# Kernel optimization log

Hardware: AMD Instinct MI355X
Metric: run time of the kernel (lower is better)

Reference implementation:

```python
import jax, jax.numpy as jnp
import numpy as np

KS = (3, 3)   # kernel_size
ST = (1, 1)   # stride
PD = (1, 1)   # padding
EPS = 1e-5


def unfold(x):
    """im2col matching torch.nn.Unfold: [B,C,H,W] -> [B, C*kh*kw, L] with (c,kh,kw) channel order, L row-major."""
    kh, kw = KS; sh, sw = ST; ph, pw = PD
    x = jnp.pad(x, ((0, 0), (0, 0), (ph, ph), (pw, pw)))
    B, C, H, W = x.shape
    Ho = (H - kh) // sh + 1
    Wo = (W - kw) // sw + 1
    I = (jnp.arange(Ho) * sh)[:, None, None, None] + jnp.arange(kh)[None, :, None, None]
    J = (jnp.arange(Wo) * sw)[None, None, :, None] + jnp.arange(kw)[None, None, None, :]
    p = x[:, :, I, J]  # [B, C, Ho, kh, Wo, kw]
    return p.transpose(0, 1, 3, 5, 2, 4).reshape(B, C * kh * kw, Ho * Wo)


def fold(cols, x_shape):
    """torch.nn.Fold is exactly the adjoint of Unfold (overlap-add)."""
    _, vjp = jax.vjp(unfold, jnp.zeros(x_shape, cols.dtype))
    return vjp(cols)[0]


def setup_inputs() -> dict:
    key = jax.random.key(0)
    k = jax.random.split(key, 6)
    B, C, H, W = 16, 64, 64, 64
    Cout, K = 64, KS[0] * KS[1]
    return {
        "x_mag": jax.random.uniform(k[0], (B, C, H, W), jnp.float32),
        "x_ang": jax.random.normal(k[1], (B, C, H, W), jnp.float32),
        "w_mag": jax.random.uniform(k[2], (C, K), jnp.float32),
        "w_ang": jax.random.uniform(k[3], (C, K), jnp.float32),
        "w1": jax.random.uniform(k[4], (C, K), jnp.float32),
        "w2": jax.random.uniform(k[5], (Cout, C), jnp.float32),
    }


def reference(x_mag, x_ang, w_mag, w_ang, w1, w2):
    B, C, H, W = x_mag.shape
    K = KS[0] * KS[1]
    Cout = w2.shape[0]
    Ho = (H + 2 * PD[0] - KS[0]) // ST[0] + 1
    Wo = (W + 2 * PD[1] - KS[1]) // ST[1] + 1

    # outer layer: unfold, mix with normalized weights, fold back (overlap-add)
    nws_mag = w_mag ** 2 / jnp.sum(w_mag ** 2)   # _normalize_weights_squared
    nw_ang = w_ang / jnp.sum(w_ang ** 2)         # _normalize_weights
    cm = unfold(x_mag).reshape(B, C, K, -1) + nws_mag[None, :, :, None]
    ca = unfold(x_ang).reshape(B, C, K, -1) * nw_ang[None, :, :, None]
    fm = fold(cm.reshape(B, C * K, -1), (B, C, H, W))
    fa = fold(ca.reshape(B, C * K, -1), (B, C, H, W))

    # helper: second unfold + weighted Frechet-mean reduction
    tbm = unfold(fm).reshape(B, C, K, -1)  # [B,C,K,L]
    tba = unfold(fa).reshape(B, C, K, -1)
    wmm1 = w1 ** 2 / jnp.sum(w1 ** 2, axis=1, keepdims=True)  # row-normalized
    wmm2 = w2 ** 2 / jnp.sum(w2 ** 2, axis=1, keepdims=True)
    wma1 = w1 ** 2 / jnp.sum(w1 ** 2)                          # globally normalized
    wma2 = w2 ** 2 / jnp.sum(w2 ** 2)

    m1 = jnp.einsum('bckl,ck->bcl', jnp.log(tbm + EPS), wmm1)
    out_mag = jnp.exp(jnp.einsum('bcl,oc->bol', m1, wmm2)).reshape(B, Cout, Ho, Wo)
    a1 = jnp.einsum('bckl,ck->bcl', tba, wma1)
    out_ang = jnp.einsum('bcl,oc->bol', a1, wma2).reshape(B, Cout, Ho, Wo)

    # from_polar -> stack (real, imag) on axis 1
    return jnp.stack([out_mag * jnp.cos(out_ang), out_mag * jnp.sin(out_ang)], axis=1)
```

## Files before the change

kernel.cpp:

```cpp
#include <hip/hip_runtime.h>
#include <math.h>

#define NB 16
#define NC 64
#define NL 4096
#define NCOUT 64
#define EPSF 1e-5f
#define LOG_EPSF -11.512925464970229f
#define CC 4
#define NCHUNK 16

#define FMA16(ACC, MV, W) \
  ACC[0].x = fmaf(MV.x, W.x, ACC[0].x); ACC[0].y = fmaf(MV.y, W.x, ACC[0].y); \
  ACC[0].z = fmaf(MV.z, W.x, ACC[0].z); ACC[0].w = fmaf(MV.w, W.x, ACC[0].w); \
  ACC[1].x = fmaf(MV.x, W.y, ACC[1].x); ACC[1].y = fmaf(MV.y, W.y, ACC[1].y); \
  ACC[1].z = fmaf(MV.z, W.y, ACC[1].z); ACC[1].w = fmaf(MV.w, W.y, ACC[1].w); \
  ACC[2].x = fmaf(MV.x, W.z, ACC[2].x); ACC[2].y = fmaf(MV.y, W.z, ACC[2].y); \
  ACC[2].z = fmaf(MV.z, W.z, ACC[2].z); ACC[2].w = fmaf(MV.w, W.z, ACC[2].w); \
  ACC[3].x = fmaf(MV.x, W.w, ACC[3].x); ACC[3].y = fmaf(MV.y, W.w, ACC[3].y); \
  ACC[3].z = fmaf(MV.z, W.w, ACC[3].z); ACC[3].w = fmaf(MV.w, W.w, ACC[3].w);

__global__ __launch_bounds__(256, 2) void fused_kernel(
    const float* __restrict__ x_mag, const float* __restrict__ x_ang,
    const float* __restrict__ wm, const float* __restrict__ wa,
    const float* __restrict__ w1, const float* __restrict__ w2,
    float* __restrict__ out)
{
    __shared__ __align__(16) float lfm[CC][4][72];
    __shared__ __align__(16) float fas[CC][4][72];
    __shared__ __align__(16) float m1r[2][CC][2][64];
    __shared__ __align__(16) float a1r[2][CC][2][64];
    __shared__ __align__(16) float w2m[64][68];
    __shared__ __align__(16) float w2a[64][68];
    __shared__ float wm1s[64][9], wa1s[64][9];
    __shared__ float smag_s[64][9], tang_s[64][9];
    __shared__ float red[4][4];

    const int tid  = threadIdx.x;
    const int lane = tid & 63;
    const int wv   = tid >> 6;

    const int bid = (blockIdx.x & 7) * 64 + (blockIdx.x >> 3);
    const int b  = bid >> 5;
    const int i0 = (bid & 31) * 2;

    const int r  = lane >> 4;
    const int j4 = lane & 15;
    const int ir = i0 - 1 + r;
    const bool ok = ((unsigned)ir < 64u);
    const int irc = ok ? ir : 0;
    const int ci = (ir == 0) ? 0 : ((ir == 63) ? 2 : 1);
    const int kL = ci * 3 + 0, kC = ci * 3 + 1, kR = ci * 3 + 2;
    const float ni = (ci == 1) ? 3.f : 2.f;
    const float nC = 3.f * ni;
    const float n0 = (j4 == 0)  ? 2.f * ni : nC;
    const float n3 = (j4 == 15) ? 2.f * ni : nC;

    const float* spm = x_mag + ((size_t)(b * NC + wv) * NL + irc * 64 + j4 * 4);
    const float* spa = x_ang + ((size_t)(b * NC + wv) * NL + irc * 64 + j4 * 4);

    float4 pfm = *(const float4*)spm;
    float4 pfa = *(const float4*)spa;

    float p0 = 0.f, p1 = 0.f, p2 = 0.f;
    {
        float v;
        v = wm[tid];       p0 += v * v;  v = wm[tid + 256]; p0 += v * v;
        v = wa[tid];       p1 += v * v;  v = wa[tid + 256]; p1 += v * v;
        v = w1[tid];       p2 += v * v;  v = w1[tid + 256]; p2 += v * v;
        if (tid < 64) {
            v = wm[tid + 512]; p0 += v * v;
            v = wa[tid + 512]; p1 += v * v;
            v = w1[tid + 512]; p2 += v * v;
        }
    }
    #pragma unroll
    for (int s = 32; s; s >>= 1) {
        p0 += __shfl_down(p0, s); p1 += __shfl_down(p1, s); p2 += __shfl_down(p2, s);
    }
    if (lane == 0) { red[0][wv] = p0; red[1][wv] = p1; red[2][wv] = p2; }

    float sqv[4][4], r2v[4][4];
    float s22p = 0.f;
    #pragma unroll
    for (int k = 0; k < 4; ++k) {
        const int oq = wv + 4 * k;
        #pragma unroll
        for (int n = 0; n < 4; ++n) {
            float v = w2[(oq * 4 + n) * 64 + lane];
            float s = v * v;
            sqv[k][n] = s;
            float rr = s;
            rr += __shfl_xor(rr, 1);  rr += __shfl_xor(rr, 2);
            rr += __shfl_xor(rr, 4);  rr += __shfl_xor(rr, 8);
            rr += __shfl_xor(rr, 16); rr += __shfl_xor(rr, 32);
            r2v[k][n] = rr;
        }
        s22p += r2v[k][0] + r2v[k][1] + r2v[k][2] + r2v[k][3];
    }
    if (lane == 0) red[3][wv] = s22p;
    __syncthreads();
    const float s_wm2 = red[0][0] + red[0][1] + red[0][2] + red[0][3];
    const float s_wa2 = red[1][0] + red[1][1] + red[1][2] + red[1][3];
    const float s_w12 = red[2][0] + red[2][1] + red[2][2] + red[2][3];
    const float inv_s22 = 1.f / (red[3][0] + red[3][1] + red[3][2] + red[3][3]);

    #pragma unroll
    for (int k = 0; k < 4; ++k) {
        const int oq = wv + 4 * k;
        float4 wmv4, wav4;
        wmv4.x = sqv[k][0] / r2v[k][0];  wav4.x = sqv[k][0] * inv_s22;
        wmv4.y = sqv[k][1] / r2v[k][1];  wav4.y = sqv[k][1] * inv_s22;
        wmv4.z = sqv[k][2] / r2v[k][2];  wav4.z = sqv[k][2] * inv_s22;
        wmv4.w = sqv[k][3] / r2v[k][3];  wav4.w = sqv[k][3] * inv_s22;
        *(float4*)&w2m[lane][oq * 4] = wmv4;
        *(float4*)&w2a[lane][oq * 4] = wav4;
    }

    if (tid < 64) {
        const int c = tid;
        float q[9]; float r1c = 0.f;
        #pragma unroll
        for (int k = 0; k < 9; ++k) { float v = w1[c * 9 + k]; q[k] = v * v; r1c += q[k]; }
        float inv_r = 1.f / r1c, inv_s = 1.f / s_w12;
        #pragma unroll
        for (int k = 0; k < 9; ++k) { wm1s[c][k] = q[k] * inv_r; wa1s[c][k] = q[k] * inv_s; }
    } else if (tid < 128) {
        const int c = tid - 64;
        float nm[9], na[9];
        const float inv_m = 1.f / s_wm2, inv_a = 1.f / s_wa2;
        #pragma unroll
        for (int k = 0; k < 9; ++k) {
            float v = wm[c * 9 + k];
            nm[k] = v * v * inv_m;
            na[k] = wa[c * 9 + k] * inv_a;
        }
        #pragma unroll
        for (int ci_ = 0; ci_ < 3; ++ci_) {
            #pragma unroll
            for (int cj = 0; cj < 3; ++cj) {
                float sm = 0.f, sa = 0.f;
                #pragma unroll
                for (int ki = 0; ki < 3; ++ki) {
                    bool vi = (ci_ == 0) ? (ki < 2) : ((ci_ == 2) ? (ki > 0) : true);
                    if (!vi) continue;
                    #pragma unroll
                    for (int kj = 0; kj < 3; ++kj) {
                        bool vj = (cj == 0) ? (kj < 2) : ((cj == 2) ? (kj > 0) : true);
                        if (!vj) continue;
                        sm += nm[ki * 3 + kj];
                        sa += na[ki * 3 + kj];
                    }
                }
                smag_s[c][ci_ * 3 + cj] = sm;
                tang_s[c][ci_ * 3 + cj] = sa;
            }
        }
    }
    __syncthreads();

    const int l0 = (tid & 15) * 4;
    const int o0 = (tid >> 4) * 4;

    float4 accm[2][4], acca[2][4];
    #pragma unroll
    for (int rr = 0; rr < 2; ++rr)
        #pragma unroll
        for (int oi = 0; oi < 4; ++oi) {
            accm[rr][oi].x = accm[rr][oi].y = accm[rr][oi].z = accm[rr][oi].w = 0.f;
            acca[rr][oi].x = acca[rr][oi].y = acca[rr][oi].z = acca[rr][oi].w = 0.f;
        }

    auto do_matmul = [&](int chm, int pp) {
        const int c0 = chm * CC;
        #pragma unroll
        for (int cc = 0; cc < CC; ++cc) {
            float4 mv0 = *(const float4*)&m1r[pp][cc][0][l0];
            float4 mv1 = *(const float4*)&m1r[pp][cc][1][l0];
            float4 av0 = *(const float4*)&a1r[pp][cc][0][l0];
            float4 av1 = *(const float4*)&a1r[pp][cc][1][l0];
            float4 wmv = *(const float4*)&w2m[c0 + cc][o0];
            float4 wav = *(const float4*)&w2a[c0 + cc][o0];
            FMA16(accm[0], mv0, wmv);
            FMA16(accm[1], mv1, wmv);
            FMA16(acca[0], av0, wav);
            FMA16(acca[1], av1, wav);
        }
    };

    #pragma unroll 2
    for (int ch = 0; ch < NCHUNK; ++ch) {
        const int p = ch & 1;

        if (ch > 0) do_matmul(ch - 1, p ^ 1);

        {
            const int cg = ch * CC + wv;
            float4 dm, da;
            if (ok) {
                float sC = smag_s[cg][kC], tC = tang_s[cg][kC];
                float s0 = (j4 == 0)  ? smag_s[cg][kL] : sC;
                float s3 = (j4 == 15) ? smag_s[cg][kR] : sC;
                float t0 = (j4 == 0)  ? tang_s[cg][kL] : tC;
                float t3 = (j4 == 15) ? tang_s[cg][kR] : tC;
                dm.x = __logf(fmaf(n0, pfm.x, s0) + EPSF);
                dm.y = __logf(fmaf(nC, pfm.y, sC) + EPSF);
                dm.z = __logf(fmaf(nC, pfm.z, sC) + EPSF);
                dm.w = __logf(fmaf(n3, pfm.w, s3) + EPSF);
                da.x = pfa.x * t0; da.y = pfa.y * tC;
                da.z = pfa.z * tC; da.w = pfa.w * t3;
            } else {
                dm.x = dm.y = dm.z = dm.w = LOG_EPSF;
                da.x = da.y = da.z = da.w = 0.f;
            }
            *(float4*)&lfm[wv][r][4 + j4 * 4] = dm;
            *(float4*)&fas[wv][r][4 + j4 * 4] = da;
            if (j4 == 0)  { lfm[wv][r][3]  = LOG_EPSF; fas[wv][r][3]  = 0.f; }
            if (j4 == 15) { lfm[wv][r][68] = LOG_EPSF; fas[wv][r][68] = 0.f; }
        }

        if (ch + 1 < NCHUNK) {
            pfm = *(const float4*)(spm + (size_t)(ch + 1) * CC * NL);
            pfa = *(const float4*)(spa + (size_t)(ch + 1) * CC * NL);
        }

        {
            const int cg = ch * CC + wv;
            float mres0 = 0.f, mres1 = 0.f, ares0 = 0.f, ares1 = 0.f;
            #pragma unroll
            for (int r_ = 0; r_ < 4; ++r_) {
                float l0v = lfm[wv][r_][lane + 3];
                float l1v = lfm[wv][r_][lane + 4];
                float l2v = lfm[wv][r_][lane + 5];
                float a0v = fas[wv][r_][lane + 3];
                float a1v = fas[wv][r_][lane + 4];
                float a2v = fas[wv][r_][lane + 5];
                if (r_ < 3) {
                    mres0 = fmaf(wm1s[cg][r_ * 3 + 0], l0v, mres0);
                    mres0 = fmaf(wm1s[cg][r_ * 3 + 1], l1v, mres0);
                    mres0 = fmaf(wm1s[cg][r_ * 3 + 2], l2v, mres0);
                    ares0 = fmaf(wa1s[cg][r_ * 3 + 0], a0v, ares0);
                    ares0 = fmaf(wa1s[cg][r_ * 3 + 1], a1v, ares0);
                    ares0 = fmaf(wa1s[cg][r_ * 3 + 2], a2v, ares0);
                }
                if (r_ > 0) {
                    const int ki = r_ - 1;
                    mres1 = fmaf(wm1s[cg][ki * 3 + 0], l0v, mres1);
                    mres1 = fmaf(wm1s[cg][ki * 3 + 1], l1v, mres1);
                    mres1 = fmaf(wm1s[cg][ki * 3 + 2], l2v, mres1);
                    ares1 = fmaf(wa1s[cg][ki * 3 + 0], a0v, ares1);
                    ares1 = fmaf(wa1s[cg][ki * 3 + 1], a1v, ares1);
                    ares1 = fmaf(wa1s[cg][ki * 3 + 2], a2v, ares1);
                }
            }
            m1r[p][wv][0][lane] = mres0;
            m1r[p][wv][1][lane] = mres1;
            a1r[p][wv][0][lane] = ares0;
            a1r[p][wv][1][lane] = ares1;
        }
        __syncthreads();
    }
    do_matmul(NCHUNK - 1, 1);

    #pragma unroll
    for (int rr = 0; rr < 2; ++rr) {
        #pragma unroll
        for (int oi = 0; oi < 4; ++oi) {
            float4 am = accm[rr][oi], aa = acca[rr][oi];
            float4 oc, os;
            float ex;
            ex = __expf(am.x); oc.x = ex * __cosf(aa.x); os.x = ex * __sinf(aa.x);
            ex = __expf(am.y); oc.y = ex * __cosf(aa.y); os.y = ex * __sinf(aa.y);
            ex = __expf(am.z); oc.z = ex * __cosf(aa.z); os.z = ex * __sinf(aa.z);
            ex = __expf(am.w); oc.w = ex * __cosf(aa.w); os.w = ex * __sinf(aa.w);
            size_t gi = ((size_t)(b * 2) * NCOUT + o0 + oi) * NL + (size_t)(i0 + rr) * 64 + l0;
            *(float4*)&out[gi] = oc;
            *(float4*)&out[gi + (size_t)NCOUT * NL] = os;
        }
    }
}

extern "C" void kernel_launch(void* const* d_in, const int* in_sizes, int n_in,
                              void* d_out, int out_size, void* d_ws, size_t ws_size,
                              hipStream_t stream) {
    const float* x_mag = (const float*)d_in[0];
    const float* x_ang = (const float*)d_in[1];
    const float* w_mag = (const float*)d_in[2];
    const float* w_ang = (const float*)d_in[3];
    const float* w1    = (const float*)d_in[4];
    const float* w2    = (const float*)d_in[5];
    float* out = (float*)d_out;

    fused_kernel<<<NB * 32, 256, 0, stream>>>(x_mag, x_ang, w_mag, w_ang, w1, w2, out);
}
```

Before: 39.99 us.

## Vectorize stencil stage and retile channel-mix matmul per thread

```diff
diff --git a/kernel.cpp b/kernel.cpp
--- a/kernel.cpp
+++ b/kernel.cpp
@@ -11,14 +11,14 @@
 #define NCHUNK 16
 
 #define FMA16(ACC, MV, W) \
-  ACC[0].x = fmaf(MV.x, W.x, ACC[0].x); ACC[0].y = fmaf(MV.y, W.x, ACC[0].y); \
-  ACC[0].z = fmaf(MV.z, W.x, ACC[0].z); ACC[0].w = fmaf(MV.w, W.x, ACC[0].w); \
-  ACC[1].x = fmaf(MV.x, W.y, ACC[1].x); ACC[1].y = fmaf(MV.y, W.y, ACC[1].y); \
-  ACC[1].z = fmaf(MV.z, W.y, ACC[1].z); ACC[1].w = fmaf(MV.w, W.y, ACC[1].w); \
-  ACC[2].x = fmaf(MV.x, W.z, ACC[2].x); ACC[2].y = fmaf(MV.y, W.z, ACC[2].y); \
-  ACC[2].z = fmaf(MV.z, W.z, ACC[2].z); ACC[2].w = fmaf(MV.w, W.z, ACC[2].w); \
-  ACC[3].x = fmaf(MV.x, W.w, ACC[3].x); ACC[3].y = fmaf(MV.y, W.w, ACC[3].y); \
-  ACC[3].z = fmaf(MV.z, W.w, ACC[3].z); ACC[3].w = fmaf(MV.w, W.w, ACC[3].w);
+  (ACC)[0].x = fmaf((MV).x,(W).x,(ACC)[0].x); (ACC)[0].y = fmaf((MV).y,(W).x,(ACC)[0].y); \
+  (ACC)[0].z = fmaf((MV).z,(W).x,(ACC)[0].z); (ACC)[0].w = fmaf((MV).w,(W).x,(ACC)[0].w); \
+  (ACC)[1].x = fmaf((MV).x,(W).y,(ACC)[1].x); (ACC)[1].y = fmaf((MV).y,(W).y,(ACC)[1].y); \
+  (ACC)[1].z = fmaf((MV).z,(W).y,(ACC)[1].z); (ACC)[1].w = fmaf((MV).w,(W).y,(ACC)[1].w); \
+  (ACC)[2].x = fmaf((MV).x,(W).z,(ACC)[2].x); (ACC)[2].y = fmaf((MV).y,(W).z,(ACC)[2].y); \
+  (ACC)[2].z = fmaf((MV).z,(W).z,(ACC)[2].z); (ACC)[2].w = fmaf((MV).w,(W).z,(ACC)[2].w); \
+  (ACC)[3].x = fmaf((MV).x,(W).w,(ACC)[3].x); (ACC)[3].y = fmaf((MV).y,(W).w,(ACC)[3].y); \
+  (ACC)[3].z = fmaf((MV).z,(W).w,(ACC)[3].z); (ACC)[3].w = fmaf((MV).w,(W).w,(ACC)[3].w);
 
 __global__ __launch_bounds__(256, 2) void fused_kernel(
     const float* __restrict__ x_mag, const float* __restrict__ x_ang,
@@ -44,23 +44,33 @@
     const int b  = bid >> 5;
     const int i0 = (bid & 31) * 2;
 
-    const int r  = lane >> 4;
+    const int sr = lane >> 4;
     const int j4 = lane & 15;
-    const int ir = i0 - 1 + r;
+    const int ir = i0 - 1 + sr;
     const bool ok = ((unsigned)ir < 64u);
     const int irc = ok ? ir : 0;
     const int ci = (ir == 0) ? 0 : ((ir == 63) ? 2 : 1);
     const int kL = ci * 3 + 0, kC = ci * 3 + 1, kR = ci * 3 + 2;
     const float ni = (ci == 1) ? 3.f : 2.f;
-    const float nC = 3.f * ni;
-    const float n0 = (j4 == 0)  ? 2.f * ni : nC;
-    const float n3 = (j4 == 15) ? 2.f * ni : nC;
+    const float nCt = 3.f * ni;
+    const float n0 = (j4 == 0)  ? 2.f * ni : nCt;
+    const float n3 = (j4 == 15) ? 2.f * ni : nCt;
 
     const float* spm = x_mag + ((size_t)(b * NC + wv) * NL + irc * 64 + j4 * 4);
     const float* spa = x_ang + ((size_t)(b * NC + wv) * NL + irc * 64 + j4 * 4);
 
     float4 pfm = *(const float4*)spm;
     float4 pfa = *(const float4*)spa;
+
+    const int cside = (lane >> 5) & 1;
+    const int crr   = (lane >> 4) & 1;
+    const int cj4   = lane & 15;
+    const float* lbase = cside ? &fas[wv][0][0] : &lfm[wv][0][0];
+    const float* wcbase = cside ? &wa1s[0][0] : &wm1s[0][0];
+
+    const int mrr = tid >> 7;
+    const int o0  = ((tid >> 4) & 7) * 8;
+    const int l0  = (tid & 15) * 4;
 
     float p0 = 0.f, p1 = 0.f, p2 = 0.f;
     {
@@ -90,11 +100,11 @@
             float v = w2[(oq * 4 + n) * 64 + lane];
             float s = v * v;
             sqv[k][n] = s;
-            float rr = s;
-            rr += __shfl_xor(rr, 1);  rr += __shfl_xor(rr, 2);
-            rr += __shfl_xor(rr, 4);  rr += __shfl_xor(rr, 8);
-            rr += __shfl_xor(rr, 16); rr += __shfl_xor(rr, 32);
-            r2v[k][n] = rr;
+            float rr_ = s;
+            rr_ += __shfl_xor(rr_, 1);  rr_ += __shfl_xor(rr_, 2);
+            rr_ += __shfl_xor(rr_, 4);  rr_ += __shfl_xor(rr_, 8);
+            rr_ += __shfl_xor(rr_, 16); rr_ += __shfl_xor(rr_, 32);
+            r2v[k][n] = rr_;
         }
         s22p += r2v[k][0] + r2v[k][1] + r2v[k][2] + r2v[k][3];
     }
@@ -159,43 +169,36 @@
     }
     __syncthreads();
 
-    const int l0 = (tid & 15) * 4;
-    const int o0 = (tid >> 4) * 4;
-
-    float4 accm[2][4], acca[2][4];
-    #pragma unroll
-    for (int rr = 0; rr < 2; ++rr)
-        #pragma unroll
-        for (int oi = 0; oi < 4; ++oi) {
-            accm[rr][oi].x = accm[rr][oi].y = accm[rr][oi].z = accm[rr][oi].w = 0.f;
-            acca[rr][oi].x = acca[rr][oi].y = acca[rr][oi].z = acca[rr][oi].w = 0.f;
-        }
+    float4 accm[8], acca[8];
+    #pragma unroll
+    for (int oi = 0; oi < 8; ++oi) {
+        accm[oi].x = accm[oi].y = accm[oi].z = accm[oi].w = 0.f;
+        acca[oi].x = acca[oi].y = acca[oi].z = acca[oi].w = 0.f;
+    }
 
     auto do_matmul = [&](int chm, int pp) {
         const int c0 = chm * CC;
         #pragma unroll
         for (int cc = 0; cc < CC; ++cc) {
-            float4 mv0 = *(const float4*)&m1r[pp][cc][0][l0];
-            float4 mv1 = *(const float4*)&m1r[pp][cc][1][l0];
-            float4 av0 = *(const float4*)&a1r[pp][cc][0][l0];
-            float4 av1 = *(const float4*)&a1r[pp][cc][1][l0];
-            float4 wmv = *(const float4*)&w2m[c0 + cc][o0];
-            float4 wav = *(const float4*)&w2a[c0 + cc][o0];
-            FMA16(accm[0], mv0, wmv);
-            FMA16(accm[1], mv1, wmv);
-            FMA16(acca[0], av0, wav);
-            FMA16(acca[1], av1, wav);
+            float4 mv  = *(const float4*)&m1r[pp][cc][mrr][l0];
+            float4 av  = *(const float4*)&a1r[pp][cc][mrr][l0];
+            float4 wm0 = *(const float4*)&w2m[c0 + cc][o0];
+            float4 wm1 = *(const float4*)&w2m[c0 + cc][o0 + 4];
+            float4 wa0 = *(const float4*)&w2a[c0 + cc][o0];
+            float4 wa1 = *(const float4*)&w2a[c0 + cc][o0 + 4];
+            FMA16((&accm[0]), mv, wm0);
+            FMA16((&accm[4]), mv, wm1);
+            FMA16((&acca[0]), av, wa0);
+            FMA16((&acca[4]), av, wa1);
         }
     };
 
     #pragma unroll 2
     for (int ch = 0; ch < NCHUNK; ++ch) {
         const int p = ch & 1;
-
-        if (ch > 0) do_matmul(ch - 1, p ^ 1);
+        const int cg = ch * CC + wv;
 
         {
-            const int cg = ch * CC + wv;
             float4 dm, da;
             if (ok) {
                 float sC = smag_s[cg][kC], tC = tang_s[cg][kC];
@@ -203,20 +206,20 @@
                 float s3 = (j4 == 15) ? smag_s[cg][kR] : sC;
                 float t0 = (j4 == 0)  ? tang_s[cg][kL] : tC;
                 float t3 = (j4 == 15) ? tang_s[cg][kR] : tC;
-                dm.x = __logf(fmaf(n0, pfm.x, s0) + EPSF);
-                dm.y = __logf(fmaf(nC, pfm.y, sC) + EPSF);
-                dm.z = __logf(fmaf(nC, pfm.z, sC) + EPSF);
-                dm.w = __logf(fmaf(n3, pfm.w, s3) + EPSF);
+                dm.x = __logf(fmaf(n0,  pfm.x, s0) + EPSF);
+                dm.y = __logf(fmaf(nCt, pfm.y, sC) + EPSF);
+                dm.z = __logf(fmaf(nCt, pfm.z, sC) + EPSF);
+                dm.w = __logf(fmaf(n3,  pfm.w, s3) + EPSF);
                 da.x = pfa.x * t0; da.y = pfa.y * tC;
                 da.z = pfa.z * tC; da.w = pfa.w * t3;
             } else {
                 dm.x = dm.y = dm.z = dm.w = LOG_EPSF;
                 da.x = da.y = da.z = da.w = 0.f;
             }
-            *(float4*)&lfm[wv][r][4 + j4 * 4] = dm;
-            *(float4*)&fas[wv][r][4 + j4 * 4] = da;
-            if (j4 == 0)  { lfm[wv][r][3]  = LOG_EPSF; fas[wv][r][3]  = 0.f; }
-            if (j4 == 15) { lfm[wv][r][68] = LOG_EPSF; fas[wv][r][68] = 0.f; }
+            *(float4*)&lfm[wv][sr][4 + j4 * 4] = dm;
+            *(float4*)&fas[wv][sr][4 + j4 * 4] = da;
+            if (j4 == 0)  { lfm[wv][sr][3]  = LOG_EPSF; fas[wv][sr][3]  = 0.f; }
+            if (j4 == 15) { lfm[wv][sr][68] = LOG_EPSF; fas[wv][sr][68] = 0.f; }
         }
 
         if (ch + 1 < NCHUNK) {
@@ -224,59 +227,61 @@
             pfa = *(const float4*)(spa + (size_t)(ch + 1) * CC * NL);
         }
 
+        if (ch > 0) do_matmul(ch - 1, p ^ 1);
+
         {
-            const int cg = ch * CC + wv;
-            float mres0 = 0.f, mres1 = 0.f, ares0 = 0.f, ares1 = 0.f;
-            #pragma unroll
-            for (int r_ = 0; r_ < 4; ++r_) {
-                float l0v = lfm[wv][r_][lane + 3];
-                float l1v = lfm[wv][r_][lane + 4];
-                float l2v = lfm[wv][r_][lane + 5];
-                float a0v = fas[wv][r_][lane + 3];
-                float a1v = fas[wv][r_][lane + 4];
-                float a2v = fas[wv][r_][lane + 5];
-                if (r_ < 3) {
-                    mres0 = fmaf(wm1s[cg][r_ * 3 + 0], l0v, mres0);
-                    mres0 = fmaf(wm1s[cg][r_ * 3 + 1], l1v, mres0);
-                    mres0 = fmaf(wm1s[cg][r_ * 3 + 2], l2v, mres0);
-                    ares0 = fmaf(wa1s[cg][r_ * 3 + 0], a0v, ares0);
-                    ares0 = fmaf(wa1s[cg][r_ * 3 + 1], a1v, ares0);
-                    ares0 = fmaf(wa1s[cg][r_ * 3 + 2], a2v, ares0);
-                }
-                if (r_ > 0) {
-                    const int ki = r_ - 1;
-                    mres1 = fmaf(wm1s[cg][ki * 3 + 0], l0v, mres1);
-                    mres1 = fmaf(wm1s[cg][ki * 3 + 1], l1v, mres1);
-                    mres1 = fmaf(wm1s[cg][ki * 3 + 2], l2v, mres1);
-                    ares1 = fmaf(wa1s[cg][ki * 3 + 0], a0v, ares1);
-                    ares1 = fmaf(wa1s[cg][ki * 3 + 1], a1v, ares1);
-                    ares1 = fmaf(wa1s[cg][ki * 3 + 2], a2v, ares1);
-                }
-            }
-            m1r[p][wv][0][lane] = mres0;
-            m1r[p][wv][1][lane] = mres1;
-            a1r[p][wv][0][lane] = ares0;
-            a1r[p][wv][1][lane] = ares1;
+            const float* kw = wcbase + cg * 9;
+            const float k0 = kw[0], k1 = kw[1], k2 = kw[2];
+            const float k3 = kw[3], k4 = kw[4], k5 = kw[5];
+            const float k6 = kw[6], k7 = kw[7], k8 = kw[8];
+            const float* srow = lbase + crr * 72 + cj4 * 4;
+            float4 L0 = *(const float4*)(srow);
+            float4 M0 = *(const float4*)(srow + 4);
+            float4 R0 = *(const float4*)(srow + 8);
+            float4 L1 = *(const float4*)(srow + 72);
+            float4 M1 = *(const float4*)(srow + 76);
+            float4 R1 = *(const float4*)(srow + 80);
+            float4 L2 = *(const float4*)(srow + 144);
+            float4 M2 = *(const float4*)(srow + 148);
+            float4 R2 = *(const float4*)(srow + 152);
+            float4 o;
+            o.x = k0 * L0.w;                 o.y = k0 * M0.x;
+            o.z = k0 * M0.y;                 o.w = k0 * M0.z;
+            o.x = fmaf(k1, M0.x, o.x);       o.y = fmaf(k1, M0.y, o.y);
+            o.z = fmaf(k1, M0.z, o.z);       o.w = fmaf(k1, M0.w, o.w);
+            o.x = fmaf(k2, M0.y, o.x);       o.y = fmaf(k2, M0.z, o.y);
+            o.z = fmaf(k2, M0.w, o.z);       o.w = fmaf(k2, R0.x, o.w);
+            o.x = fmaf(k3, L1.w, o.x);       o.y = fmaf(k3, M1.x, o.y);
+            o.z = fmaf(k3, M1.y, o.z);       o.w = fmaf(k3, M1.z, o.w);
+            o.x = fmaf(k4, M1.x, o.x);       o.y = fmaf(k4, M1.y, o.y);
+            o.z = fmaf(k4, M1.z, o.z);       o.w = fmaf(k4, M1.w, o.w);
+            o.x = fmaf(k5, M1.y, o.x);       o.y = fmaf(k5, M1.z, o.y);
+            o.z = fmaf(k5, M1.w, o.z);       o.w = fmaf(k5, R1.x, o.w);
+            o.x = fmaf(k6, L2.w, o.x);       o.y = fmaf(k6, M2.x, o.y);
+            o.z = fmaf(k6, M2.y, o.z);       o.w = fmaf(k6, M2.z, o.w);
+            o.x = fmaf(k7, M2.x, o.x);       o.y = fmaf(k7, M2.y, o.y);
+            o.z = fmaf(k7, M2.z, o.z);       o.w = fmaf(k7, M2.w, o.w);
+            o.x = fmaf(k8, M2.y, o.x);       o.y = fmaf(k8, M2.z, o.y);
+            o.z = fmaf(k8, M2.w, o.z);       o.w = fmaf(k8, R2.x, o.w);
+            float* dst = cside ? &a1r[p][wv][crr][0] : &m1r[p][wv][crr][0];
+            *(float4*)(dst + cj4 * 4) = o;
         }
         __syncthreads();
     }
     do_matmul(NCHUNK - 1, 1);
 
     #pragma unroll
-    for (int rr = 0; rr < 2; ++rr) {
-        #pragma unroll
-        for (int oi = 0; oi < 4; ++oi) {
-            float4 am = accm[rr][oi], aa = acca[rr][oi];
-            float4 oc, os;
-            float ex;
-            ex = __expf(am.x); oc.x = ex * __cosf(aa.x); os.x = ex * __sinf(aa.x);
-            ex = __expf(am.y); oc.y = ex * __cosf(aa.y); os.y = ex * __sinf(aa.y);
-            ex = __expf(am.z); oc.z = ex * __cosf(aa.z); os.z = ex * __sinf(aa.z);
-            ex = __expf(am.w); oc.w = ex * __cosf(aa.w); os.w = ex * __sinf(aa.w);
-            size_t gi = ((size_t)(b * 2) * NCOUT + o0 + oi) * NL + (size_t)(i0 + rr) * 64 + l0;
-            *(float4*)&out[gi] = oc;
-            *(float4*)&out[gi + (size_t)NCOUT * NL] = os;
-        }
+    for (int oi = 0; oi < 8; ++oi) {
+        float4 am = accm[oi], aa = acca[oi];
+        float4 oc, os;
+        float ex;
+        ex = __expf(am.x); oc.x = ex * __cosf(aa.x); os.x = ex * __sinf(aa.x);
+        ex = __expf(am.y); oc.y = ex * __cosf(aa.y); os.y = ex * __sinf(aa.y);
+        ex = __expf(am.z); oc.z = ex * __cosf(aa.z); os.z = ex * __sinf(aa.z);
+        ex = __expf(am.w); oc.w = ex * __cosf(aa.w); os.w = ex * __sinf(aa.w);
+        size_t gi = ((size_t)(b * 2) * NCOUT + o0 + oi) * NL + (size_t)(i0 + mrr) * 64 + l0;
+        *(float4*)&out[gi] = oc;
+        *(float4*)&out[gi + (size_t)NCOUT * NL] = os;
     }
 }
 
```

Measured after the change: 43.69 us. 9.3% more time.

## Double block threads, factor angle weights into per-row scale, drop w2a tile

Applied to the files above, without the earlier changes.

```diff
diff --git a/kernel.cpp b/kernel.cpp
--- a/kernel.cpp
+++ b/kernel.cpp
@@ -7,20 +7,20 @@
 #define NCOUT 64
 #define EPSF 1e-5f
 #define LOG_EPSF -11.512925464970229f
-#define CC 4
-#define NCHUNK 16
+#define CC 8
+#define NCHUNK 8
 
 #define FMA16(ACC, MV, W) \
-  ACC[0].x = fmaf(MV.x, W.x, ACC[0].x); ACC[0].y = fmaf(MV.y, W.x, ACC[0].y); \
-  ACC[0].z = fmaf(MV.z, W.x, ACC[0].z); ACC[0].w = fmaf(MV.w, W.x, ACC[0].w); \
-  ACC[1].x = fmaf(MV.x, W.y, ACC[1].x); ACC[1].y = fmaf(MV.y, W.y, ACC[1].y); \
-  ACC[1].z = fmaf(MV.z, W.y, ACC[1].z); ACC[1].w = fmaf(MV.w, W.y, ACC[1].w); \
-  ACC[2].x = fmaf(MV.x, W.z, ACC[2].x); ACC[2].y = fmaf(MV.y, W.z, ACC[2].y); \
-  ACC[2].z = fmaf(MV.z, W.z, ACC[2].z); ACC[2].w = fmaf(MV.w, W.z, ACC[2].w); \
-  ACC[3].x = fmaf(MV.x, W.w, ACC[3].x); ACC[3].y = fmaf(MV.y, W.w, ACC[3].y); \
-  ACC[3].z = fmaf(MV.z, W.w, ACC[3].z); ACC[3].w = fmaf(MV.w, W.w, ACC[3].w);
-
-__global__ __launch_bounds__(256, 2) void fused_kernel(
+  (ACC)[0].x = fmaf((MV).x,(W).x,(ACC)[0].x); (ACC)[0].y = fmaf((MV).y,(W).x,(ACC)[0].y); \
+  (ACC)[0].z = fmaf((MV).z,(W).x,(ACC)[0].z); (ACC)[0].w = fmaf((MV).w,(W).x,(ACC)[0].w); \
+  (ACC)[1].x = fmaf((MV).x,(W).y,(ACC)[1].x); (ACC)[1].y = fmaf((MV).y,(W).y,(ACC)[1].y); \
+  (ACC)[1].z = fmaf((MV).z,(W).y,(ACC)[1].z); (ACC)[1].w = fmaf((MV).w,(W).y,(ACC)[1].w); \
+  (ACC)[2].x = fmaf((MV).x,(W).z,(ACC)[2].x); (ACC)[2].y = fmaf((MV).y,(W).z,(ACC)[2].y); \
+  (ACC)[2].z = fmaf((MV).z,(W).z,(ACC)[2].z); (ACC)[2].w = fmaf((MV).w,(W).z,(ACC)[2].w); \
+  (ACC)[3].x = fmaf((MV).x,(W).w,(ACC)[3].x); (ACC)[3].y = fmaf((MV).y,(W).w,(ACC)[3].y); \
+  (ACC)[3].z = fmaf((MV).z,(W).w,(ACC)[3].z); (ACC)[3].w = fmaf((MV).w,(W).w,(ACC)[3].w);
+
+__global__ __launch_bounds__(512, 4) void fused_kernel(
     const float* __restrict__ x_mag, const float* __restrict__ x_ang,
     const float* __restrict__ wm, const float* __restrict__ wa,
     const float* __restrict__ w1, const float* __restrict__ w2,
@@ -31,10 +31,10 @@
     __shared__ __align__(16) float m1r[2][CC][2][64];
     __shared__ __align__(16) float a1r[2][CC][2][64];
     __shared__ __align__(16) float w2m[64][68];
-    __shared__ __align__(16) float w2a[64][68];
     __shared__ float wm1s[64][9], wa1s[64][9];
     __shared__ float smag_s[64][9], tang_s[64][9];
-    __shared__ float red[4][4];
+    __shared__ float red[4][8];
+    __shared__ __align__(16) float rho[64];
 
     const int tid  = threadIdx.x;
     const int lane = tid & 63;
@@ -44,30 +44,34 @@
     const int b  = bid >> 5;
     const int i0 = (bid & 31) * 2;
 
-    const int r  = lane >> 4;
+    const int sr = lane >> 4;
     const int j4 = lane & 15;
-    const int ir = i0 - 1 + r;
+    const int ir = i0 - 1 + sr;
     const bool ok = ((unsigned)ir < 64u);
     const int irc = ok ? ir : 0;
     const int ci = (ir == 0) ? 0 : ((ir == 63) ? 2 : 1);
     const int kL = ci * 3 + 0, kC = ci * 3 + 1, kR = ci * 3 + 2;
     const float ni = (ci == 1) ? 3.f : 2.f;
-    const float nC = 3.f * ni;
-    const float n0 = (j4 == 0)  ? 2.f * ni : nC;
-    const float n3 = (j4 == 15) ? 2.f * ni : nC;
+    const float nCt = 3.f * ni;
+    const float n0 = (j4 == 0)  ? 2.f * ni : nCt;
+    const float n3 = (j4 == 15) ? 2.f * ni : nCt;
 
     const float* spm = x_mag + ((size_t)(b * NC + wv) * NL + irc * 64 + j4 * 4);
     const float* spa = x_ang + ((size_t)(b * NC + wv) * NL + irc * 64 + j4 * 4);
 
     float4 pfm = *(const float4*)spm;
     float4 pfa = *(const float4*)spa;
+
+    const int mrr = tid >> 8;
+    const int o0  = ((tid >> 4) & 15) * 4;
+    const int l0  = (tid & 15) * 4;
 
     float p0 = 0.f, p1 = 0.f, p2 = 0.f;
     {
         float v;
-        v = wm[tid];       p0 += v * v;  v = wm[tid + 256]; p0 += v * v;
-        v = wa[tid];       p1 += v * v;  v = wa[tid + 256]; p1 += v * v;
-        v = w1[tid];       p2 += v * v;  v = w1[tid + 256]; p2 += v * v;
+        v = wm[tid]; p0 += v * v;
+        v = wa[tid]; p1 += v * v;
+        v = w1[tid]; p2 += v * v;
         if (tid < 64) {
             v = wm[tid + 512]; p0 += v * v;
             v = wa[tid + 512]; p1 += v * v;
@@ -80,41 +84,50 @@
     }
     if (lane == 0) { red[0][wv] = p0; red[1][wv] = p1; red[2][wv] = p2; }
 
-    float sqv[4][4], r2v[4][4];
+    float sqv[2][4], r2v[2][4];
     float s22p = 0.f;
     #pragma unroll
-    for (int k = 0; k < 4; ++k) {
-        const int oq = wv + 4 * k;
+    for (int k = 0; k < 2; ++k) {
+        const int oq = wv + 8 * k;
         #pragma unroll
         for (int n = 0; n < 4; ++n) {
             float v = w2[(oq * 4 + n) * 64 + lane];
             float s = v * v;
             sqv[k][n] = s;
-            float rr = s;
-            rr += __shfl_xor(rr, 1);  rr += __shfl_xor(rr, 2);
-            rr += __shfl_xor(rr, 4);  rr += __shfl_xor(rr, 8);
-            rr += __shfl_xor(rr, 16); rr += __shfl_xor(rr, 32);
-            r2v[k][n] = rr;
+            float rr_ = s;
+            rr_ += __shfl_xor(rr_, 1);  rr_ += __shfl_xor(rr_, 2);
+            rr_ += __shfl_xor(rr_, 4);  rr_ += __shfl_xor(rr_, 8);
+            rr_ += __shfl_xor(rr_, 16); rr_ += __shfl_xor(rr_, 32);
+            r2v[k][n] = rr_;
         }
         s22p += r2v[k][0] + r2v[k][1] + r2v[k][2] + r2v[k][3];
     }
     if (lane == 0) red[3][wv] = s22p;
     __syncthreads();
-    const float s_wm2 = red[0][0] + red[0][1] + red[0][2] + red[0][3];
-    const float s_wa2 = red[1][0] + red[1][1] + red[1][2] + red[1][3];
-    const float s_w12 = red[2][0] + red[2][1] + red[2][2] + red[2][3];
-    const float inv_s22 = 1.f / (red[3][0] + red[3][1] + red[3][2] + red[3][3]);
-
-    #pragma unroll
-    for (int k = 0; k < 4; ++k) {
-        const int oq = wv + 4 * k;
-        float4 wmv4, wav4;
-        wmv4.x = sqv[k][0] / r2v[k][0];  wav4.x = sqv[k][0] * inv_s22;
-        wmv4.y = sqv[k][1] / r2v[k][1];  wav4.y = sqv[k][1] * inv_s22;
-        wmv4.z = sqv[k][2] / r2v[k][2];  wav4.z = sqv[k][2] * inv_s22;
-        wmv4.w = sqv[k][3] / r2v[k][3];  wav4.w = sqv[k][3] * inv_s22;
+    const float s_wm2 = red[0][0] + red[0][1] + red[0][2] + red[0][3]
+                      + red[0][4] + red[0][5] + red[0][6] + red[0][7];
+    const float s_wa2 = red[1][0] + red[1][1] + red[1][2] + red[1][3]
+                      + red[1][4] + red[1][5] + red[1][6] + red[1][7];
+    const float s_w12 = red[2][0] + red[2][1] + red[2][2] + red[2][3]
+                      + red[2][4] + red[2][5] + red[2][6] + red[2][7];
+    const float inv_s22 = 1.f / (red[3][0] + red[3][1] + red[3][2] + red[3][3]
+                               + red[3][4] + red[3][5] + red[3][6] + red[3][7]);
+
+    #pragma unroll
+    for (int k = 0; k < 2; ++k) {
+        const int oq = wv + 8 * k;
+        float4 wmv4;
+        wmv4.x = sqv[k][0] / r2v[k][0];
+        wmv4.y = sqv[k][1] / r2v[k][1];
+        wmv4.z = sqv[k][2] / r2v[k][2];
+        wmv4.w = sqv[k][3] / r2v[k][3];
         *(float4*)&w2m[lane][oq * 4] = wmv4;
-        *(float4*)&w2a[lane][oq * 4] = wav4;
+        if (lane == 0) {
+            rho[oq * 4 + 0] = r2v[k][0] * inv_s22;
+            rho[oq * 4 + 1] = r2v[k][1] * inv_s22;
+            rho[oq * 4 + 2] = r2v[k][2] * inv_s22;
+            rho[oq * 4 + 3] = r2v[k][3] * inv_s22;
+        }
     }
 
     if (tid < 64) {
@@ -159,43 +172,31 @@
     }
     __syncthreads();
 
-    const int l0 = (tid & 15) * 4;
-    const int o0 = (tid >> 4) * 4;
-
-    float4 accm[2][4], acca[2][4];
-    #pragma unroll
-    for (int rr = 0; rr < 2; ++rr)
-        #pragma unroll
-        for (int oi = 0; oi < 4; ++oi) {
-            accm[rr][oi].x = accm[rr][oi].y = accm[rr][oi].z = accm[rr][oi].w = 0.f;
-            acca[rr][oi].x = acca[rr][oi].y = acca[rr][oi].z = acca[rr][oi].w = 0.f;
-        }
+    float4 accm[4], acca[4];
+    #pragma unroll
+    for (int oi = 0; oi < 4; ++oi) {
+        accm[oi].x = accm[oi].y = accm[oi].z = accm[oi].w = 0.f;
+        acca[oi].x = acca[oi].y = acca[oi].z = acca[oi].w = 0.f;
+    }
 
     auto do_matmul = [&](int chm, int pp) {
         const int c0 = chm * CC;
         #pragma unroll
         for (int cc = 0; cc < CC; ++cc) {
-            float4 mv0 = *(const float4*)&m1r[pp][cc][0][l0];
-            float4 mv1 = *(const float4*)&m1r[pp][cc][1][l0];
-            float4 av0 = *(const float4*)&a1r[pp][cc][0][l0];
-            float4 av1 = *(const float4*)&a1r[pp][cc][1][l0];
+            float4 mv  = *(const float4*)&m1r[pp][cc][mrr][l0];
+            float4 av  = *(const float4*)&a1r[pp][cc][mrr][l0];
             float4 wmv = *(const float4*)&w2m[c0 + cc][o0];
-            float4 wav = *(const float4*)&w2a[c0 + cc][o0];
-            FMA16(accm[0], mv0, wmv);
-            FMA16(accm[1], mv1, wmv);
-            FMA16(acca[0], av0, wav);
-            FMA16(acca[1], av1, wav);
+            FMA16(accm, mv, wmv);
+            FMA16(acca, av, wmv);
         }
     };
 
     #pragma unroll 2
     for (int ch = 0; ch < NCHUNK; ++ch) {
         const int p = ch & 1;
-
-        if (ch > 0) do_matmul(ch - 1, p ^ 1);
+        const int cg = ch * CC + wv;
 
         {
-            const int cg = ch * CC + wv;
             float4 dm, da;
             if (ok) {
                 float sC = smag_s[cg][kC], tC = tang_s[cg][kC];
@@ -203,20 +204,20 @@
                 float s3 = (j4 == 15) ? smag_s[cg][kR] : sC;
                 float t0 = (j4 == 0)  ? tang_s[cg][kL] : tC;
                 float t3 = (j4 == 15) ? tang_s[cg][kR] : tC;
-                dm.x = __logf(fmaf(n0, pfm.x, s0) + EPSF);
-                dm.y = __logf(fmaf(nC, pfm.y, sC) + EPSF);
-                dm.z = __logf(fmaf(nC, pfm.z, sC) + EPSF);
-                dm.w = __logf(fmaf(n3, pfm.w, s3) + EPSF);
+                dm.x = __logf(fmaf(n0,  pfm.x, s0) + EPSF);
+                dm.y = __logf(fmaf(nCt, pfm.y, sC) + EPSF);
+                dm.z = __logf(fmaf(nCt, pfm.z, sC) + EPSF);
+                dm.w = __logf(fmaf(n3,  pfm.w, s3) + EPSF);
                 da.x = pfa.x * t0; da.y = pfa.y * tC;
                 da.z = pfa.z * tC; da.w = pfa.w * t3;
             } else {
                 dm.x = dm.y = dm.z = dm.w = LOG_EPSF;
                 da.x = da.y = da.z = da.w = 0.f;
             }
-            *(float4*)&lfm[wv][r][4 + j4 * 4] = dm;
-            *(float4*)&fas[wv][r][4 + j4 * 4] = da;
-            if (j4 == 0)  { lfm[wv][r][3]  = LOG_EPSF; fas[wv][r][3]  = 0.f; }
-            if (j4 == 15) { lfm[wv][r][68] = LOG_EPSF; fas[wv][r][68] = 0.f; }
+            *(float4*)&lfm[wv][sr][4 + j4 * 4] = dm;
+            *(float4*)&fas[wv][sr][4 + j4 * 4] = da;
+            if (j4 == 0)  { lfm[wv][sr][3]  = LOG_EPSF; fas[wv][sr][3]  = 0.f; }
+            if (j4 == 15) { lfm[wv][sr][68] = LOG_EPSF; fas[wv][sr][68] = 0.f; }
         }
 
         if (ch + 1 < NCHUNK) {
@@ -224,8 +225,9 @@
             pfa = *(const float4*)(spa + (size_t)(ch + 1) * CC * NL);
         }
 
+        if (ch > 0) do_matmul(ch - 1, p ^ 1);
+
         {
-            const int cg = ch * CC + wv;
             float mres0 = 0.f, mres1 = 0.f, ares0 = 0.f, ares1 = 0.f;
             #pragma unroll
             for (int r_ = 0; r_ < 4; ++r_) {
@@ -262,21 +264,24 @@
     }
     do_matmul(NCHUNK - 1, 1);
 
-    #pragma unroll
-    for (int rr = 0; rr < 2; ++rr) {
-        #pragma unroll
-        for (int oi = 0; oi < 4; ++oi) {
-            float4 am = accm[rr][oi], aa = acca[rr][oi];
-            float4 oc, os;
-            float ex;
-            ex = __expf(am.x); oc.x = ex * __cosf(aa.x); os.x = ex * __sinf(aa.x);
-            ex = __expf(am.y); oc.y = ex * __cosf(aa.y); os.y = ex * __sinf(aa.y);
-            ex = __expf(am.z); oc.z = ex * __cosf(aa.z); os.z = ex * __sinf(aa.z);
-            ex = __expf(am.w); oc.w = ex * __cosf(aa.w); os.w = ex * __sinf(aa.w);
-            size_t gi = ((size_t)(b * 2) * NCOUT + o0 + oi) * NL + (size_t)(i0 + rr) * 64 + l0;
-            *(float4*)&out[gi] = oc;
-            *(float4*)&out[gi + (size_t)NCOUT * NL] = os;
-        }
+    const float4 rh4 = *(const float4*)&rho[o0];
+    acca[0].x *= rh4.x; acca[0].y *= rh4.x; acca[0].z *= rh4.x; acca[0].w *= rh4.x;
+    acca[1].x *= rh4.y; acca[1].y *= rh4.y; acca[1].z *= rh4.y; acca[1].w *= rh4.y;
+    acca[2].x *= rh4.z; acca[2].y *= rh4.z; acca[2].z *= rh4.z; acca[2].w *= rh4.z;
+    acca[3].x *= rh4.w; acca[3].y *= rh4.w; acca[3].z *= rh4.w; acca[3].w *= rh4.w;
+
+    #pragma unroll
+    for (int oi = 0; oi < 4; ++oi) {
+        float4 am = accm[oi], aa = acca[oi];
+        float4 oc, os;
+        float ex;
+        ex = __expf(am.x); oc.x = ex * __cosf(aa.x); os.x = ex * __sinf(aa.x);
+        ex = __expf(am.y); oc.y = ex * __cosf(aa.y); os.y = ex * __sinf(aa.y);
+        ex = __expf(am.z); oc.z = ex * __cosf(aa.z); os.z = ex * __sinf(aa.z);
+        ex = __expf(am.w); oc.w = ex * __cosf(aa.w); os.w = ex * __sinf(aa.w);
+        size_t gi = ((size_t)(b * 2) * NCOUT + o0 + oi) * NL + (size_t)(i0 + mrr) * 64 + l0;
+        *(float4*)&out[gi] = oc;
+        *(float4*)&out[gi + (size_t)NCOUT * NL] = os;
     }
 }
 
@@ -291,5 +296,5 @@
     const float* w2    = (const float*)d_in[5];
     float* out = (float*)d_out;
 
-    fused_kernel<<<NB * 32, 256, 0, stream>>>(x_mag, x_ang, w_mag, w_ang, w1, w2, out);
+    fused_kernel<<<NB * 32, 512, 0, stream>>>(x_mag, x_ang, w_mag, w_ang, w1, w2, out);
 }
```

Result: slower. 42.59 us (+6.5%).
